# Optimization experiments

Hardware: AMD Instinct MI355X
Metric: run time of the kernel (lower is better)

The kernel has to match this reference:

```python
import jax, jax.numpy as jnp
import numpy as np

ALPHA = 0.2  # module hardcodes a = 0.2


def _triplet_total(outputs, labels):
    # Faithful vectorization of the nested-loop mining:
    #  - sort samples by label (stable, like python sorted with key=label)
    #  - anchor p1 = first element of each contiguous label group
    #  - positives p2 = remaining members of the group; ap = ||p1-p2||^2
    #  - negatives = every sample with a different label
    #  - per (p2, neg): add (ap - an + alpha) for an in {||p1-n||^2, ||p2-n||^2}
    #    iff ap < an and ap - an + alpha > 0  (i.e. 0 < an - ap < alpha)
    order = jnp.argsort(labels)          # stable sort, matches python sorted
    x = outputs[order]                   # [n, d]
    lab = labels[order]                  # [n]
    n = x.shape[0]
    idx = jnp.arange(n)
    is_start = jnp.concatenate([jnp.ones((1,), bool), lab[1:] != lab[:-1]])
    # index of the group-start (anchor) for every position
    anchor_of = jax.lax.cummax(jnp.where(is_start, idx, 0))

    # pairwise squared distances Dm[i,j] = ||x_i - x_j||^2
    sq = jnp.sum(x * x, axis=-1)                       # [n]
    Dm = sq[:, None] + sq[None, :] - 2.0 * (x @ x.T)   # [n, n]

    ap = Dm[anchor_of, idx]   # [n]   ||p1 - p2||^2 for each potential positive
    an1 = Dm[anchor_of, :]    # [n,n] ||p1 - neg||^2
    an2 = Dm                  # [n,n] ||p2 - neg||^2

    pos_mask = ~is_start                         # p2 ranges over non-anchor rows
    neg_mask = lab[:, None] != lab[None, :]      # negatives: different label
    valid = pos_mask[:, None] & neg_mask         # [n, n]

    def hinge(an):
        d = ap[:, None] - an
        return jnp.where((d < 0) & (d + ALPHA > 0), d + ALPHA, 0.0)

    contrib = jnp.where(valid, hinge(an1) + hinge(an2), 0.0)
    return jnp.sum(contrib)


def setup_inputs() -> dict:
    key = jax.random.key(0)
    k1, k2 = jax.random.split(key)
    N, D, C = 8192, 128, 512
    outputs = jax.random.normal(k1, (N, D), dtype=jnp.float32)
    labels = jax.random.randint(k2, (N,), 0, C, dtype=jnp.int32)
    return {"outputs": outputs, "labels": labels}


def reference(outputs, labels):
    return _triplet_total(outputs, labels)
```

## Files before the change

kernel.cpp:

```cpp
#include <hip/hip_runtime.h>
#include <limits.h>
#include <stdint.h>

#define ALPHA 0.2f
#define HALFA 0.1f
static constexpr int N = 8192;
static constexpr int D = 128;
static constexpr int C = 512;
static constexpr int BT = 128;
static constexpr int GR = D / 8;
static constexpr int SL = BT + 1;
static constexpr int MAXG = 48;
static constexpr int NB = N / BT;
static constexpr int NSP = NB / 2;
static constexpr int SPB = 16;
static constexpr int GRID = 512;

using half8    = __attribute__((ext_vector_type(8))) _Float16;
using floatx16 = __attribute__((ext_vector_type(16))) float;

__device__ __forceinline__ floatx16 zerov() { floatx16 v = {0.f}; return v; }

__device__ __forceinline__ half8 cvt8(float4 v0, float4 v1) {
    half8 h;
    h[0] = (_Float16)v0.x; h[1] = (_Float16)v0.y; h[2] = (_Float16)v0.z; h[3] = (_Float16)v0.w;
    h[4] = (_Float16)v1.x; h[5] = (_Float16)v1.y; h[6] = (_Float16)v1.z; h[7] = (_Float16)v1.w;
    return h;
}

__device__ __forceinline__ float ss8(float4 v0, float4 v1) {
    return v0.x*v0.x + v0.y*v0.y + v0.z*v0.z + v0.w*v0.w
         + v1.x*v1.x + v1.y*v1.y + v1.z*v1.z + v1.w*v1.w;
}

__device__ __forceinline__ void dec_sp(int k, int t, int lenA, int& br, int& bc) {
    if (t < lenA) { br = k;      bc = k + t; }
    else          { br = 63 - k; bc = 63 - k + (t - lenA); }
}


__launch_bounds__(256)
__global__ void k_prep(const float* __restrict__ x, const int* __restrict__ labels,
                       _Float16* __restrict__ xh, float* __restrict__ sq,
                       int* __restrict__ anchorg, float* __restrict__ ap,
                       int* __restrict__ ecnt, float* __restrict__ egrid,
                       float* __restrict__ out) {
    __shared__ int sAnc[C];
    const int tid = threadIdx.x;
    if (blockIdx.x == 0 && tid == 0) out[0] = 0.f;
    for (int i = tid; i < C; i += 256) sAnc[i] = INT_MAX;
    __syncthreads();
    const int4* lab4 = (const int4*)labels;
    for (int t = tid; t < N / 4; t += 256) {
        int4 lv = lab4[t];
        int base = 4 * t;
        atomicMin(&sAnc[lv.x], base);
        atomicMin(&sAnc[lv.y], base + 1);
        atomicMin(&sAnc[lv.z], base + 2);
        atomicMin(&sAnc[lv.w], base + 3);
    }
    __syncthreads();
    if (tid < 2) {
        int c = blockIdx.x * 2 + tid;
        int a = sAnc[c];
        anchorg[c] = (a == INT_MAX) ? -1 : a;
    }

    const int r = blockIdx.x * 32 + (tid >> 3);
    const int sub = tid & 7;
    const float4* src = (const float4*)(x + (size_t)r * D) + sub * 4;
    half8* dst = (half8*)(xh + (size_t)r * D) + sub * 2;
    half8 hj[2];
    float ssj = 0.f;
#pragma unroll
    for (int i = 0; i < 2; ++i) {
        float4 v0 = src[2 * i], v1 = src[2 * i + 1];
        hj[i] = cvt8(v0, v1);
        dst[i] = hj[i];
        ssj += ss8(v0, v1);
    }
    ssj += __shfl_xor(ssj, 1); ssj += __shfl_xor(ssj, 2); ssj += __shfl_xor(ssj, 4);

    const int lab = labels[r];
    const int a = sAnc[lab];
    const float4* asrc = (const float4*)(x + (size_t)a * D) + sub * 4;
    float ssa = 0.f, dot = 0.f;
#pragma unroll
    for (int i = 0; i < 2; ++i) {
        float4 a0 = asrc[2 * i], a1 = asrc[2 * i + 1];
        half8 ha = cvt8(a0, a1);
        ssa += ss8(a0, a1);
#pragma unroll
        for (int e = 0; e < 8; ++e) dot = fmaf((float)ha[e], (float)hj[i][e], dot);
    }
    ssa += __shfl_xor(ssa, 1); ssa += __shfl_xor(ssa, 2); ssa += __shfl_xor(ssa, 4);
    dot += __shfl_xor(dot, 1); dot += __shfl_xor(dot, 2); dot += __shfl_xor(dot, 4);
    if (sub == 0) {
        float apv = ssa + ssj - 2.f * dot;
        sq[r] = ssj;
        ap[r] = apv;
        if (r != a) {
            int slot = atomicAdd(&ecnt[lab], 1);
            if (slot < MAXG) egrid[(size_t)lab * MAXG + slot] = apv + HALFA;
        }
    }
}


__launch_bounds__(512, 2)
__global__ void k_main(const _Float16* __restrict__ xh, const int* __restrict__ labels,
                       const int* __restrict__ anchor, const float* __restrict__ sq,
                       const float* __restrict__ ap, const int* __restrict__ ecnt,
                       const float* __restrict__ egrid, float* __restrict__ out) {
    __shared__ __align__(16) _Float16 BsH[GR * SL * 8];
    __shared__ __align__(16) float sge[64 * MAXG];
    __shared__ float4 rowE[BT];
    __shared__ float4 colE[2][BT];
    __shared__ int   sArow[64];
    __shared__ float sSqA[64];
    __shared__ int   sCnt[64];
    __shared__ float wsum[8];
    half8* Bs = (half8*)BsH;

    const int tid = threadIdx.x;
    const int lane = tid & 63, w = tid >> 6;
    const int m = lane & 31, q = lane >> 5;
    const int sg = tid & 15, sr0 = tid >> 4;
    float local = 0.f;
    int cnt = 0;

    const int b = blockIdx.x;
    const int c0 = (b >> 6) * 64, j1 = (b & 63) * BT;
    const int kk_sp = b >> 4, p = b & 15;
    const int lenA = 64 - kk_sp;

    if (tid < 64) {
        int c = c0 + tid;
        int a = anchor[c];
        int ar = (a < 0) ? 0 : a;
        sArow[tid] = ar;
        sSqA[tid] = sq[ar];
        int n = ecnt[c];
        sCnt[tid] = (n > MAXG) ? MAXG : n;
    }
    {
        const float4* srcv = (const float4*)(egrid + (size_t)c0 * MAXG);
        float4* dstv = (float4*)sge;
        dstv[tid] = srcv[tid];
        if (tid < 64 * MAXG / 4 - 512) dstv[tid + 512] = srcv[tid + 512];
    }
    half8 breg[4];
#pragma unroll
    for (int i = 0; i < 4; ++i)
        breg[i] = *((const half8*)(xh + (size_t)(j1 + sr0 + 32 * i) * D) + sg);
    if (tid < BT) {
        int j = j1 + tid;
        colE[0][tid] = make_float4(sq[j], __int_as_float(labels[j]), 0.f, 0.f);
    }
    __syncthreads();

    half8 af[8];
    {
        int arow = sArow[(w >> 2) * 32 + m];
        const half8* aptr = (const half8*)(xh + (size_t)arow * D) + q;
#pragma unroll
        for (int k = 0; k < 8; ++k) af[k] = aptr[2 * k];
    }
#pragma unroll
    for (int i = 0; i < 4; ++i)
        Bs[sg * SL + sr0 + 32 * i] = breg[i];
    __syncthreads();

    floatx16 acc = zerov();
#pragma unroll
    for (int k = 0; k < 8; ++k) {
        half8 b0 = Bs[(2 * k + q) * SL + (w & 3) * 32 + m];
        acc = __builtin_amdgcn_mfma_f32_32x32x16_f16(af[k], b0, acc, 0, 0, 0);
    }

    int br0, bc0; dec_sp(kk_sp, p, lenA, br0, bc0);
    {
        const half8* aptr = (const half8*)(xh + (size_t)(br0 * BT + (w >> 1) * 32 + m) * D) + q;
#pragma unroll
        for (int k = 0; k < 8; ++k) af[k] = aptr[2 * k];
#pragma unroll
        for (int i = 0; i < 4; ++i)
            breg[i] = *((const half8*)(xh + (size_t)(bc0 * BT + sr0 + 32 * i) * D) + sg);
        if (tid < BT) {
            int i = br0 * BT + tid;
            int li = labels[i]; int a = anchor[li];
            float sqi = sq[i];
            float e2 = (i == a) ? -1e30f : ap[i] + HALFA - sqi;
            rowE[tid] = make_float4(e2, __int_as_float(li), sqi, 0.f);
        } else if (tid < 2 * BT) {
            int j = bc0 * BT + tid - BT;
            int lj = labels[j]; int a = anchor[lj];
            float sqj = sq[j];
            float e2 = (j == a) ? -1e30f : ap[j] + HALFA - sqj;
            colE[1][tid - BT] = make_float4(e2, __int_as_float(lj), sqj, 0.f);
        }
    }

    {
        float4 cj = colE[0][(w & 3) * 32 + m];
        float sqj = cj.x; int labj = __float_as_int(cj.y);
#pragma unroll
        for (int rr = 0; rr < 16; ++rr) {
            int row = (w >> 2) * 32 + (rr & 3) + 8 * (rr >> 2) + 4 * q;
            float Dv = fmaf(-2.f, acc[rr], sSqA[row] + sqj);
            Dv = (labj != c0 + row) ? Dv : 3.0e38f;
            int nf = (sCnt[row] + 3) & ~3;
            cnt += nf;
            for (int gb = 0; gb < nf; gb += 4) {
                float4 ev = *(const float4*)&sge[row * MAXG + gb];
                float u;
                u = ev.x - Dv; local += (__builtin_fabsf(u) < HALFA) ? u : -HALFA;
                u = ev.y - Dv; local += (__builtin_fabsf(u) < HALFA) ? u : -HALFA;
                u = ev.z - Dv; local += (__builtin_fabsf(u) < HALFA) ? u : -HALFA;
                u = ev.w - Dv; local += (__builtin_fabsf(u) < HALFA) ? u : -HALFA;
            }
        }
    }
    __syncthreads();

    {
        const int wr = w >> 1, wc = w & 1;
        int cbuf = 1, cur_br = br0;

        for (int t = p; t < 65; t += SPB) {
            int br, bc; dec_sp(kk_sp, t, lenA, br, bc);
            const int i0 = br * BT;
            const bool diag = (br == bc);

            if (br != cur_br) {
                cur_br = br;
                const half8* aptr = (const half8*)(xh + (size_t)(i0 + wr * 32 + m) * D) + q;
#pragma unroll
                for (int k8 = 0; k8 < 8; ++k8) af[k8] = aptr[2 * k8];
                if (tid < BT) {
                    int i = i0 + tid;
                    int li = labels[i]; int a = anchor[li];
                    float sqi = sq[i];
                    float e2 = (i == a) ? -1e30f : ap[i] + HALFA - sqi;
                    rowE[tid] = make_float4(e2, __int_as_float(li), sqi, 0.f);
                }
            }

#pragma unroll
            for (int i = 0; i < 4; ++i)
                Bs[sg * SL + sr0 + 32 * i] = breg[i];
            __syncthreads();

            if (t + SPB < 65) {
                int brn, bcn; dec_sp(kk_sp, t + SPB, lenA, brn, bcn);
                int j0n = bcn * BT;
#pragma unroll
                for (int i = 0; i < 4; ++i)
                    breg[i] = *((const half8*)(xh + (size_t)(j0n + sr0 + 32 * i) * D) + sg);
                if (tid < BT) {
                    int j = j0n + tid;
                    int lj = labels[j]; int a = anchor[lj];
                    float sqj = sq[j];
                    float e2 = (j == a) ? -1e30f : ap[j] + HALFA - sqj;
                    colE[cbuf ^ 1][tid] = make_float4(e2, __int_as_float(lj), sqj, 0.f);
                }
            }

            floatx16 acc0 = zerov(), acc1 = zerov();
#pragma unroll
            for (int k8 = 0; k8 < 8; ++k8) {
                half8 b0 = Bs[(2 * k8 + q) * SL + wc * 64 + m];
                half8 b1 = Bs[(2 * k8 + q) * SL + wc * 64 + 32 + m];
                acc0 = __builtin_amdgcn_mfma_f32_32x32x16_f16(af[k8], b0, acc0, 0, 0, 0);
                acc1 = __builtin_amdgcn_mfma_f32_32x32x16_f16(af[k8], b1, acc1, 0, 0, 0);
            }

            float sqjv[2], e2j[2]; int labj[2];
            { float4 cj = colE[cbuf][wc * 64 + m];      e2j[0] = cj.x; labj[0] = __float_as_int(cj.y); sqjv[0] = cj.z; }
            { float4 cj = colE[cbuf][wc * 64 + 32 + m]; e2j[1] = cj.x; labj[1] = __float_as_int(cj.y); sqjv[1] = cj.z; }

#pragma unroll
            for (int rr = 0; rr < 16; ++rr) {
                int row = wr * 32 + (rr & 3) + 8 * (rr >> 2) + 4 * q;
                float4 re = rowE[row];
                float e2i = re.x, sqi = re.z;
                int labi = __float_as_int(re.y);
#pragma unroll
                for (int tn = 0; tn < 2; ++tn) {
                    float dot = (tn == 0) ? acc0[rr] : acc1[rr];
                    bool ne = (labi != labj[tn]);
                    float b1v = ne ? (e2i - sqjv[tn]) : 3.0e38f;
                    float u2 = fmaf(2.f, dot, b1v);
                    local += (__builtin_fabsf(u2) < HALFA) ? u2 : -HALFA;
                    if (!diag) {
                        float b2v = ne ? (e2j[tn] - sqi) : 3.0e38f;
                        float u2b = fmaf(2.f, dot, b2v);
                        local += (__builtin_fabsf(u2b) < HALFA) ? u2b : -HALFA;
                    }
                }
            }
            cnt += diag ? 32 : 64;
            cbuf ^= 1;
            __syncthreads();
        }
    }

    local += HALFA * (float)cnt;
#pragma unroll
    for (int off = 32; off; off >>= 1) local += __shfl_down(local, off);
    if (lane == 0) wsum[w] = local;
    __syncthreads();
    if (tid == 0) {
        float s = 0.f;
#pragma unroll
        for (int i = 0; i < 8; ++i) s += wsum[i];
        atomicAdd(out, s);
    }
}


extern "C" void kernel_launch(void* const* d_in, const int* in_sizes, int n_in,
                              void* d_out, int out_size, void* d_ws, size_t ws_size,
                              hipStream_t stream) {
    const float* x = (const float*)d_in[0];
    const int* labels = (const int*)d_in[1];
    float* out = (float*)d_out;

    char* p = (char*)d_ws;
    int* anchor = (int*)p;        p += C * 4;
    float* sq = (float*)p;        p += N * 4;
    float* ap = (float*)p;        p += N * 4;
    int* ecnt = (int*)p;          p += C * 4;
    float* egrid = (float*)p;     p += (size_t)C * MAXG * 4;
    p = (char*)(((uintptr_t)p + 255) & ~(uintptr_t)255);
    _Float16* xh = (_Float16*)p;

    hipMemsetAsync(ecnt, 0, C * 4, stream);
    hipMemsetAsync(egrid, 0x7F, (size_t)C * MAXG * 4, stream);
    k_prep<<<N / 32, 256, 0, stream>>>(x, labels, xh, sq, anchor, ap, ecnt, egrid, out);
    k_main<<<GRID, 512, 0, stream>>>(xh, labels, anchor, sq, ap, ecnt, egrid, out);
}
```

Measured before the change: 107.4 us.

## Rebalance triangle tile schedule across 768 blocks and drop egrid memset

Replaces the paired-row triangle schedule (512 blocks, strided tiles) with a linear triangle enumeration split over 768 blocks. The first 512 blocks do the anchor-side phase plus 2 tiles, and the remaining blocks take 4 or 5 tiles each, to even out per-block work. Shared-memory padding of unused egrid slots now happens at load time, so the 0x7F memset is removed. In exchange it adds a serial loop to decode the start tile index and introduces uneven tile counts per block.

```diff
diff --git a/kernel.cpp b/kernel.cpp
--- a/kernel.cpp
+++ b/kernel.cpp
@@ -12,9 +12,12 @@
 static constexpr int SL = BT + 1;
 static constexpr int MAXG = 48;
 static constexpr int NB = N / BT;
-static constexpr int NSP = NB / 2;
-static constexpr int SPB = 16;
-static constexpr int GRID = 512;
+static constexpr int NT1T = 512;
+static constexpr int NTRI = NB * (NB + 1) / 2;
+static constexpr int GRID = 768;
+
+#define DMASK 3.0e38f
+#define EPAD  1.0e37f
 
 using half8    = __attribute__((ext_vector_type(8))) _Float16;
 using floatx16 = __attribute__((ext_vector_type(16))) float;
@@ -31,11 +34,6 @@
 __device__ __forceinline__ float ss8(float4 v0, float4 v1) {
     return v0.x*v0.x + v0.y*v0.y + v0.z*v0.z + v0.w*v0.w
          + v1.x*v1.x + v1.y*v1.y + v1.z*v1.z + v1.w*v1.w;
-}
-
-__device__ __forceinline__ void dec_sp(int k, int t, int lenA, int& br, int& bc) {
-    if (t < lenA) { br = k;      bc = k + t; }
-    else          { br = 63 - k; bc = 63 - k + (t - lenA); }
 }
 
 
@@ -130,56 +128,77 @@
     int cnt = 0;
 
     const int b = blockIdx.x;
+    const bool hasT1 = (b < NT1T);
     const int c0 = (b >> 6) * 64, j1 = (b & 63) * BT;
-    const int kk_sp = b >> 4, p = b & 15;
-    const int lenA = 64 - kk_sp;
-
-    if (tid < 64) {
-        int c = c0 + tid;
-        int a = anchor[c];
-        int ar = (a < 0) ? 0 : a;
-        sArow[tid] = ar;
-        sSqA[tid] = sq[ar];
-        int n = ecnt[c];
-        sCnt[tid] = (n > MAXG) ? MAXG : n;
-    }
+    int ts, te;
+    if (b < 512)      { ts = 2 * b;                te = ts + 2; }
+    else if (b < 736) { ts = 1024 + (b - 512) * 4; te = ts + 4; }
+    else              { ts = 1920 + (b - 736) * 5; te = ts + 5; }
+
+    half8 af[8], breg[4];
+    floatx16 acc = zerov();
+
+    if (hasT1) {
+        if (tid < 64) {
+            int c = c0 + tid;
+            int a = anchor[c];
+            int ar = (a < 0) ? 0 : a;
+            sArow[tid] = ar;
+            sSqA[tid] = sq[ar];
+            int n = ecnt[c];
+            sCnt[tid] = (n > MAXG) ? MAXG : n;
+        }
+        {
+            const float4* srcv = (const float4*)(egrid + (size_t)c0 * MAXG);
+            float4* dstv = (float4*)sge;
+#pragma unroll
+            for (int rep = 0; rep < 2; ++rep) {
+                int idx = tid + rep * 512;
+                if (idx < 64 * (MAXG / 4)) {
+                    int cls = idx / (MAXG / 4);
+                    int sb = (idx % (MAXG / 4)) * 4;
+                    int n = ecnt[c0 + cls]; n = (n > MAXG) ? MAXG : n;
+                    float4 v = srcv[idx];
+                    v.x = (sb + 0 < n) ? v.x : EPAD;
+                    v.y = (sb + 1 < n) ? v.y : EPAD;
+                    v.z = (sb + 2 < n) ? v.z : EPAD;
+                    v.w = (sb + 3 < n) ? v.w : EPAD;
+                    dstv[idx] = v;
+                }
+            }
+        }
+#pragma unroll
+        for (int i = 0; i < 4; ++i)
+            breg[i] = *((const half8*)(xh + (size_t)(j1 + sr0 + 32 * i) * D) + sg);
+        if (tid < BT) {
+            int j = j1 + tid;
+            colE[0][tid] = make_float4(sq[j], __int_as_float(labels[j]), 0.f, 0.f);
+        }
+        __syncthreads();
+
+        {
+            int arow = sArow[(w >> 2) * 32 + m];
+            const half8* aptr = (const half8*)(xh + (size_t)arow * D) + q;
+#pragma unroll
+            for (int k = 0; k < 8; ++k) af[k] = aptr[2 * k];
+        }
+#pragma unroll
+        for (int i = 0; i < 4; ++i)
+            Bs[sg * SL + sr0 + 32 * i] = breg[i];
+        __syncthreads();
+
+#pragma unroll
+        for (int k = 0; k < 8; ++k) {
+            half8 b0 = Bs[(2 * k + q) * SL + (w & 3) * 32 + m];
+            acc = __builtin_amdgcn_mfma_f32_32x32x16_f16(af[k], b0, acc, 0, 0, 0);
+        }
+    }
+
+    int br0 = 0;
     {
-        const float4* srcv = (const float4*)(egrid + (size_t)c0 * MAXG);
-        float4* dstv = (float4*)sge;
-        dstv[tid] = srcv[tid];
-        if (tid < 64 * MAXG / 4 - 512) dstv[tid + 512] = srcv[tid + 512];
-    }
-    half8 breg[4];
-#pragma unroll
-    for (int i = 0; i < 4; ++i)
-        breg[i] = *((const half8*)(xh + (size_t)(j1 + sr0 + 32 * i) * D) + sg);
-    if (tid < BT) {
-        int j = j1 + tid;
-        colE[0][tid] = make_float4(sq[j], __int_as_float(labels[j]), 0.f, 0.f);
-    }
-    __syncthreads();
-
-    half8 af[8];
-    {
-        int arow = sArow[(w >> 2) * 32 + m];
-        const half8* aptr = (const half8*)(xh + (size_t)arow * D) + q;
-#pragma unroll
-        for (int k = 0; k < 8; ++k) af[k] = aptr[2 * k];
-    }
-#pragma unroll
-    for (int i = 0; i < 4; ++i)
-        Bs[sg * SL + sr0 + 32 * i] = breg[i];
-    __syncthreads();
-
-    floatx16 acc = zerov();
-#pragma unroll
-    for (int k = 0; k < 8; ++k) {
-        half8 b0 = Bs[(2 * k + q) * SL + (w & 3) * 32 + m];
-        acc = __builtin_amdgcn_mfma_f32_32x32x16_f16(af[k], b0, acc, 0, 0, 0);
-    }
-
-    int br0, bc0; dec_sp(kk_sp, p, lenA, br0, bc0);
-    {
+        int rem = ts;
+        while (rem >= NB - br0) { rem -= NB - br0; ++br0; }
+        int bc0 = br0 + rem;
         const half8* aptr = (const half8*)(xh + (size_t)(br0 * BT + (w >> 1) * 32 + m) * D) + q;
 #pragma unroll
         for (int k = 0; k < 8; ++k) af[k] = aptr[2 * k];
@@ -201,14 +220,14 @@
         }
     }
 
-    {
+    if (hasT1) {
         float4 cj = colE[0][(w & 3) * 32 + m];
         float sqj = cj.x; int labj = __float_as_int(cj.y);
 #pragma unroll
         for (int rr = 0; rr < 16; ++rr) {
             int row = (w >> 2) * 32 + (rr & 3) + 8 * (rr >> 2) + 4 * q;
             float Dv = fmaf(-2.f, acc[rr], sSqA[row] + sqj);
-            Dv = (labj != c0 + row) ? Dv : 3.0e38f;
+            Dv = (labj != c0 + row) ? Dv : DMASK;
             int nf = (sCnt[row] + 3) & ~3;
             cnt += nf;
             for (int gb = 0; gb < nf; gb += 4) {
@@ -226,9 +245,14 @@
     {
         const int wr = w >> 1, wc = w & 1;
         int cbuf = 1, cur_br = br0;
-
-        for (int t = p; t < 65; t += SPB) {
-            int br, bc; dec_sp(kk_sp, t, lenA, br, bc);
+        int br = br0, bc = br0;
+        {
+            int rem = ts, brx = 0;
+            while (rem >= NB - brx) { rem -= NB - brx; ++brx; }
+            bc = brx + rem;
+        }
+
+        for (int t = ts; t < te; ++t) {
             const int i0 = br * BT;
             const bool diag = (br == bc);
 
@@ -251,8 +275,9 @@
                 Bs[sg * SL + sr0 + 32 * i] = breg[i];
             __syncthreads();
 
-            if (t + SPB < 65) {
-                int brn, bcn; dec_sp(kk_sp, t + SPB, lenA, brn, bcn);
+            int brn = br, bcn = bc + 1;
+            if (bcn == NB) { ++brn; bcn = brn; }
+            if (t + 1 < te) {
                 int j0n = bcn * BT;
 #pragma unroll
                 for (int i = 0; i < 4; ++i)
@@ -289,17 +314,18 @@
                 for (int tn = 0; tn < 2; ++tn) {
                     float dot = (tn == 0) ? acc0[rr] : acc1[rr];
                     bool ne = (labi != labj[tn]);
-                    float b1v = ne ? (e2i - sqjv[tn]) : 3.0e38f;
+                    float b1v = ne ? (e2i - sqjv[tn]) : DMASK;
                     float u2 = fmaf(2.f, dot, b1v);
                     local += (__builtin_fabsf(u2) < HALFA) ? u2 : -HALFA;
                     if (!diag) {
-                        float b2v = ne ? (e2j[tn] - sqi) : 3.0e38f;
+                        float b2v = ne ? (e2j[tn] - sqi) : DMASK;
                         float u2b = fmaf(2.f, dot, b2v);
                         local += (__builtin_fabsf(u2b) < HALFA) ? u2b : -HALFA;
                     }
                 }
             }
             cnt += diag ? 32 : 64;
+            br = brn; bc = bcn;
             cbuf ^= 1;
             __syncthreads();
         }
@@ -336,7 +362,6 @@
     _Float16* xh = (_Float16*)p;
 
     hipMemsetAsync(ecnt, 0, C * 4, stream);
-    hipMemsetAsync(egrid, 0x7F, (size_t)C * MAXG * 4, stream);
     k_prep<<<N / 32, 256, 0, stream>>>(x, labels, xh, sq, anchor, ap, ecnt, egrid, out);
     k_main<<<GRID, 512, 0, stream>>>(xh, labels, anchor, sq, ap, ecnt, egrid, out);
 }
```

New measurement: 115.1 us. +7.2%, slower.

## Drop egrid memset by padding in-kernel; add setprio around MFMA/epilogue

Applied to the files above, without the earlier changes.

Removes the hipMemsetAsync that filled egrid with large values. Instead, unused slots are padded with a large constant when the grid is loaded into shared memory, based on ecnt. It also wraps the compute sections with s_setprio to raise wave priority, and folds the label-mismatch mask into the hinge predicate rather than selecting a sentinel. Together these remove one launch and a few selects per element, at the cost of extra ecnt reads and index math during the shared-memory fill.

```diff
diff --git a/kernel.cpp b/kernel.cpp
--- a/kernel.cpp
+++ b/kernel.cpp
@@ -12,9 +12,13 @@
 static constexpr int SL = BT + 1;
 static constexpr int MAXG = 48;
 static constexpr int NB = N / BT;
+static constexpr int NT1T = 512;
 static constexpr int NSP = NB / 2;
 static constexpr int SPB = 16;
 static constexpr int GRID = 512;
+
+#define DMASK 3.0e38f
+#define EPAD  1.0e37f
 
 using half8    = __attribute__((ext_vector_type(8))) _Float16;
 using floatx16 = __attribute__((ext_vector_type(16))) float;
@@ -134,6 +138,9 @@
     const int kk_sp = b >> 4, p = b & 15;
     const int lenA = 64 - kk_sp;
 
+    half8 af[8], breg[4];
+    floatx16 acc = zerov();
+
     if (tid < 64) {
         int c = c0 + tid;
         int a = anchor[c];
@@ -146,10 +153,22 @@
     {
         const float4* srcv = (const float4*)(egrid + (size_t)c0 * MAXG);
         float4* dstv = (float4*)sge;
-        dstv[tid] = srcv[tid];
-        if (tid < 64 * MAXG / 4 - 512) dstv[tid + 512] = srcv[tid + 512];
-    }
-    half8 breg[4];
+#pragma unroll
+        for (int rep = 0; rep < 2; ++rep) {
+            int idx = tid + rep * 512;
+            if (idx < 64 * (MAXG / 4)) {
+                int cls = idx / (MAXG / 4);
+                int sb = (idx % (MAXG / 4)) * 4;
+                int n = ecnt[c0 + cls]; n = (n > MAXG) ? MAXG : n;
+                float4 v = srcv[idx];
+                v.x = (sb + 0 < n) ? v.x : EPAD;
+                v.y = (sb + 1 < n) ? v.y : EPAD;
+                v.z = (sb + 2 < n) ? v.z : EPAD;
+                v.w = (sb + 3 < n) ? v.w : EPAD;
+                dstv[idx] = v;
+            }
+        }
+    }
 #pragma unroll
     for (int i = 0; i < 4; ++i)
         breg[i] = *((const half8*)(xh + (size_t)(j1 + sr0 + 32 * i) * D) + sg);
@@ -159,7 +178,6 @@
     }
     __syncthreads();
 
-    half8 af[8];
     {
         int arow = sArow[(w >> 2) * 32 + m];
         const half8* aptr = (const half8*)(xh + (size_t)arow * D) + q;
@@ -171,14 +189,14 @@
         Bs[sg * SL + sr0 + 32 * i] = breg[i];
     __syncthreads();
 
-    floatx16 acc = zerov();
 #pragma unroll
     for (int k = 0; k < 8; ++k) {
         half8 b0 = Bs[(2 * k + q) * SL + (w & 3) * 32 + m];
         acc = __builtin_amdgcn_mfma_f32_32x32x16_f16(af[k], b0, acc, 0, 0, 0);
     }
 
-    int br0, bc0; dec_sp(kk_sp, p, lenA, br0, bc0);
+    int br0, bc0;
+    dec_sp(kk_sp, p, lenA, br0, bc0);
     {
         const half8* aptr = (const half8*)(xh + (size_t)(br0 * BT + (w >> 1) * 32 + m) * D) + q;
 #pragma unroll
@@ -201,6 +219,7 @@
         }
     }
 
+    __builtin_amdgcn_s_setprio(1);
     {
         float4 cj = colE[0][(w & 3) * 32 + m];
         float sqj = cj.x; int labj = __float_as_int(cj.y);
@@ -208,7 +227,7 @@
         for (int rr = 0; rr < 16; ++rr) {
             int row = (w >> 2) * 32 + (rr & 3) + 8 * (rr >> 2) + 4 * q;
             float Dv = fmaf(-2.f, acc[rr], sSqA[row] + sqj);
-            Dv = (labj != c0 + row) ? Dv : 3.0e38f;
+            Dv = (labj != c0 + row) ? Dv : DMASK;
             int nf = (sCnt[row] + 3) & ~3;
             cnt += nf;
             for (int gb = 0; gb < nf; gb += 4) {
@@ -221,6 +240,7 @@
             }
         }
     }
+    __builtin_amdgcn_s_setprio(0);
     __syncthreads();
 
     {
@@ -266,6 +286,7 @@
                 }
             }
 
+            __builtin_amdgcn_s_setprio(1);
             floatx16 acc0 = zerov(), acc1 = zerov();
 #pragma unroll
             for (int k8 = 0; k8 < 8; ++k8) {
@@ -289,16 +310,15 @@
                 for (int tn = 0; tn < 2; ++tn) {
                     float dot = (tn == 0) ? acc0[rr] : acc1[rr];
                     bool ne = (labi != labj[tn]);
-                    float b1v = ne ? (e2i - sqjv[tn]) : 3.0e38f;
-                    float u2 = fmaf(2.f, dot, b1v);
-                    local += (__builtin_fabsf(u2) < HALFA) ? u2 : -HALFA;
+                    float u2 = fmaf(2.f, dot, e2i - sqjv[tn]);
+                    local += (ne & (__builtin_fabsf(u2) < HALFA)) ? u2 : -HALFA;
                     if (!diag) {
-                        float b2v = ne ? (e2j[tn] - sqi) : 3.0e38f;
-                        float u2b = fmaf(2.f, dot, b2v);
-                        local += (__builtin_fabsf(u2b) < HALFA) ? u2b : -HALFA;
+                        float u2b = fmaf(2.f, dot, e2j[tn] - sqi);
+                        local += (ne & (__builtin_fabsf(u2b) < HALFA)) ? u2b : -HALFA;
                     }
                 }
             }
+            __builtin_amdgcn_s_setprio(0);
             cnt += diag ? 32 : 64;
             cbuf ^= 1;
             __syncthreads();
@@ -336,7 +356,6 @@
     _Float16* xh = (_Float16*)p;
 
     hipMemsetAsync(ecnt, 0, C * 4, stream);
-    hipMemsetAsync(egrid, 0x7F, (size_t)C * MAXG * 4, stream);
     k_prep<<<N / 32, 256, 0, stream>>>(x, labels, xh, sq, anchor, ap, ecnt, egrid, out);
     k_main<<<GRID, 512, 0, stream>>>(xh, labels, anchor, sq, ap, ecnt, egrid, out);
 }
```

Result: faster. 105.1 us (-2.1%).
